# Optimization experiments

Measured on AMD Instinct MI355X. Metric: run time of the kernel, lower is better.

The kernel has to match this reference:

```python
import jax, jax.numpy as jnp
import numpy as np

H = 128      # hidden_size
L = 2        # num_layers
IN0 = 96     # seq_feature_size + context_feature_size
OUT = 1

def _xavier(k, shape):
    fan_out, fan_in = shape
    lim = (6.0 / (fan_in + fan_out)) ** 0.5
    return jax.random.uniform(k, shape, jnp.float32, -lim, lim)

def _orth(k, n):
    q, _ = jnp.linalg.qr(jax.random.normal(k, (n, n)))
    return q.astype(jnp.float32)

def setup_inputs() -> dict:
    key = jax.random.key(0)
    ks = jax.random.split(key, 16)
    B, S, F_seq, F_ctx = 512, 512, 64, 32
    inp = {
        "seq_features": jax.random.normal(ks[0], (B, S, F_seq), jnp.float32),
        "context_features": jax.random.normal(ks[1], (B, F_ctx), jnp.float32),
    }
    for i in range(L):
        in_size = IN0 if i == 0 else H
        inp[f"tau{i}"] = jax.random.normal(ks[2 + 5 * i], (H,), jnp.float32) * 0.1
        inp[f"Win{i}"] = _xavier(ks[3 + 5 * i], (H, in_size))
        inp[f"Wrec{i}"] = _orth(ks[4 + 5 * i], H)
        inp[f"Wg{i}"] = _xavier(ks[5 + 5 * i], (H, in_size + H))
        inp[f"bg{i}"] = jnp.zeros((H,), jnp.float32)
    inp["W1"] = _xavier(ks[12], (H // 2, H))
    inp["b1"] = jnp.zeros((H // 2,), jnp.float32)
    inp["W2"] = _xavier(ks[13], (OUT, H // 2))
    inp["b2"] = jnp.zeros((OUT,), jnp.float32)
    return inp

def _cell_step(x, h, tau_p, Win, Wrec, Wg, bg):
    # LTC cell: RK4 integration of dh/dt = -h/tau + W_in x + gate * W_rec h
    tau = jax.nn.softplus(tau_p) + 1.0
    def rhs(hh):
        gate = jax.nn.sigmoid(jnp.tanh(jnp.concatenate([x, hh], axis=-1) @ Wg.T + bg))
        return -hh / tau + x @ Win.T + gate * (hh @ Wrec.T)
    k1 = rhs(h)
    k2 = rhs(h + 0.5 * k1)
    k3 = rhs(h + 0.5 * k2)
    k4 = rhs(h + k3)
    return jnp.tanh(h + (k1 + 2.0 * k2 + 2.0 * k3 + k4) / 6.0)

def reference(seq_features, context_features, tau0, Win0, Wrec0, Wg0, bg0,
              tau1, Win1, Wrec1, Wg1, bg1, W1, b1, W2, b2):
    B, S, _ = seq_features.shape
    ctx = jnp.broadcast_to(context_features[:, None, :], (B, S, context_features.shape[-1]))
    x = jnp.concatenate([seq_features, ctx], axis=-1)     # [B,S,IN0]
    xs = jnp.swapaxes(x, 0, 1)                            # [S,B,IN0] time-major
    cells = [(tau0, Win0, Wrec0, Wg0, bg0), (tau1, Win1, Wrec1, Wg1, bg1)]
    h_init = tuple(jnp.zeros((B, H), x.dtype) for _ in range(L))

    def step(hs, xt):
        new = []
        inp = xt
        for hi, p in zip(hs, cells):
            hn = _cell_step(inp, hi, *p)
            new.append(hn)
            inp = hn
        return tuple(new), None

    hs, _ = jax.lax.scan(step, h_init, xs)
    h_last = hs[-1]                                       # [B,H]
    # classifier (dropout is identity in eval mode)
    out = jax.nn.sigmoid(jax.nn.relu(h_last @ W1.T + b1) @ W2.T + b2)
    return out.reshape(B, -1)
```

## Files before the change

kernel.cpp:

```cpp
#include <hip/hip_runtime.h>


typedef _Float16 f16;
typedef _Float16 f16x4 __attribute__((ext_vector_type(4)));
typedef _Float16 f16x8 __attribute__((ext_vector_type(8)));
typedef float f32x2 __attribute__((ext_vector_type(2)));
typedef float f32x4 __attribute__((ext_vector_type(4)));

#define NSTEP 512
#define OFF_A0 0
#define OFF_A1 32768
#define OFF_AIO 65536
#define OFF_AX 98304
#define W_TOTAL 122880

#define HQ0 0
#define HQ1 4352
#define L0A 8704
#define L0B 13056
#define L1A 17408
#define L1B 21760
#define L1H 26112
#define XT0 30464
#define XT1 32768
#define SMEM_BYTES 35072

__device__ __forceinline__ float rcp_f(float x) { return __builtin_amdgcn_rcpf(x); }

#define FMA2(A, B, C) __builtin_elementwise_fma((A), (B), (C))
#define B2(X) ((f32x2){(X), (X)})
#define ZERO4 ((f32x4){0.f, 0.f, 0.f, 0.f})
#define ZERO2 ((f32x2){0.f, 0.f})

__device__ __forceinline__ f32x2 tanh2_f(f32x2 z) {
  f32x2 zz = z + z;
  f32x2 e = {__expf(zz[0]), __expf(zz[1])};
  f32x2 d = e + 1.f;
  f32x2 r = {rcp_f(d[0]), rcp_f(d[1])};
  return FMA2(r, B2(-2.f), B2(1.f));
}
__device__ __forceinline__ f32x2 sig2_f(f32x2 t) {
  f32x2 s = t * t;
  f32x2 p = FMA2(s, B2(2.1356861e-5f), B2(-2.1081349e-4f));
  p = FMA2(s, p, B2(2.0833333e-3f));
  p = FMA2(s, p, B2(-2.0833333e-2f));
  p = FMA2(s, p, B2(0.25f));
  return FMA2(t, p, B2(0.5f));
}

#define BAR()                                            \
  do {                                                   \
    asm volatile("s_waitcnt lgkmcnt(0)" ::: "memory");   \
    __builtin_amdgcn_s_barrier();                        \
  } while (0)

__global__ __launch_bounds__(256) void prep_kernel(
    const float* __restrict__ Win0, const float* __restrict__ Wrec0,
    const float* __restrict__ Wg0, const float* __restrict__ Win1,
    const float* __restrict__ Wrec1, const float* __restrict__ Wg1,
    f16* __restrict__ W) {
  int i = blockIdx.x * 256 + threadIdx.x;
  if (i >= W_TOTAL) return;
  if (i < OFF_AX) {
    int sec = i >> 15;
    int r = i & 32767;
    int j = r & 7, lane = (r >> 3) & 63, kc = (r >> 9) & 3, sel = (r >> 11) & 1,
        w = (r >> 12) & 7;
    int row = w * 16 + (lane & 15);
    int k = kc * 32 + ((lane >> 4) << 3) + j;
    float v;
    if (sec == 0)
      v = sel ? Wrec0[row * 128 + k] : Wg0[row * 224 + 96 + k];
    else if (sec == 1)
      v = sel ? Wrec1[row * 128 + k] : Wg1[row * 256 + 128 + k];
    else
      v = sel ? Wg1[row * 256 + k] : Win1[row * 128 + k];
    W[i] = (f16)v;
  } else {
    int r = i - OFF_AX;
    int j = r & 7, lane = (r >> 3) & 63, g = r >> 9;
    int kc = g % 3, sg = g / 3;
    int sel = sg & 1, w = sg >> 1;
    int row = w * 16 + (lane & 15);
    int k = kc * 32 + ((lane >> 4) << 3) + j;
    W[i] = (f16)(sel ? Wg0[row * 224 + k] : Win0[row * 96 + k]);
  }
}

#define MFMA16(A, B, C) __builtin_amdgcn_mfma_f32_16x16x32_f16((A), (B), (C), 0, 0, 0)

#define MM2G(SRC)                                                   \
  {                                                                 \
    ga[0] = gx4[0]; ga[1] = gx4[1];                                 \
    ra[0] = ZERO4; ra[1] = ZERO4;                                   \
    const f16* bp_ = (SRC) + c * 136 + 8 * q;                       \
    _Pragma("unroll") for (int kc_ = 0; kc_ < 4; ++kc_) {           \
      f16x8 bf_ = *(const f16x8*)(bp_ + kc_ * 32);                  \
      ga[0] = MFMA16(awg[0][kc_], bf_, ga[0]);                      \
      ra[0] = MFMA16(awr[0][kc_], bf_, ra[0]);                      \
      ga[1] = MFMA16(awg[1][kc_], bf_, ga[1]);                      \
      ra[1] = MFMA16(awr[1][kc_], bf_, ra[1]);                      \
    }                                                               \
  }

#define MMIO_B(SRC)                                                 \
  {                                                                 \
    ga[0] = ZERO4; ga[1] = ZERO4;                                   \
    ra[0] = bgv4[0]; ra[1] = bgv4[1];                               \
    const f16* bp_ = (SRC) + c * 136 + 8 * q;                       \
    _Pragma("unroll") for (int kc_ = 0; kc_ < 4; ++kc_) {           \
      f16x8 bf_ = *(const f16x8*)(bp_ + kc_ * 32);                  \
      ga[0] = MFMA16(au[0][kc_], bf_, ga[0]);                       \
      ra[0] = MFMA16(ag2[0][kc_], bf_, ra[0]);                      \
      ga[1] = MFMA16(au[1][kc_], bf_, ga[1]);                       \
      ra[1] = MFMA16(ag2[1][kc_], bf_, ra[1]);                      \
    }                                                               \
  }

#define XPROJ(XSRC, UD, GD)                                         \
  {                                                                 \
    f32x4 tg_[2], tr_[2];                                           \
    tg_[0] = ZERO4; tg_[1] = ZERO4;                                 \
    tr_[0] = bgv4[0]; tr_[1] = bgv4[1];                             \
    f16x8 bx0_ = *(const f16x8*)((XSRC) + c * 72 + 8 * q);          \
    f16x8 bx1_ = *(const f16x8*)((XSRC) + c * 72 + 32 + 8 * q);     \
    _Pragma("unroll") for (int i2_ = 0; i2_ < 2; ++i2_) {           \
      tg_[i2_] = MFMA16(au[i2_][0], bx0_, tg_[i2_]);                \
      tr_[i2_] = MFMA16(ag2[i2_][0], bx0_, tr_[i2_]);               \
      tg_[i2_] = MFMA16(au[i2_][1], bx1_, tg_[i2_]);                \
      tr_[i2_] = MFMA16(ag2[i2_][1], bx1_, tr_[i2_]);               \
      tg_[i2_] = MFMA16(au[i2_][2], bctx, tg_[i2_]);                \
      tr_[i2_] = MFMA16(ag2[i2_][2], bctx, tr_[i2_]);               \
      (UD)[i2_] = tg_[i2_];                                         \
      (GD)[i2_] = tr_[i2_];                                         \
    }                                                               \
  }

#define GATEP(WC, HC, DST, FIRST)                                   \
  _Pragma("unroll") for (int i2_ = 0; i2_ < 2; ++i2_) {             \
    f16x4 hv_;                                                      \
    _Pragma("unroll") for (int p_ = 0; p_ < 2; ++p_) {              \
      f32x2 z_ = p_ ? (f32x2){ga[i2_][2], ga[i2_][3]}               \
                    : (f32x2){ga[i2_][0], ga[i2_][1]};              \
      f32x2 rr_ = p_ ? (f32x2){ra[i2_][2], ra[i2_][3]}              \
                     : (f32x2){ra[i2_][0], ra[i2_][1]};             \
      f32x2 th_ = tanh2_f(z_);                                      \
      f32x2 gt_ = sig2_f(th_);                                      \
      f32x2 kk_ = FMA2(gt_, rr_,                                    \
                       FMA2(nitv2[i2_][p_], hhc2[i2_][p_], u2[i2_][p_])); \
      ksum2[i2_][p_] = (FIRST) ? kk_ : FMA2(B2(WC), kk_, ksum2[i2_][p_]); \
      f32x2 hn_ = FMA2(B2(HC), kk_, hst2[i2_][p_]);                 \
      hhc2[i2_][p_] = hn_;                                          \
      hv_[2 * p_] = (f16)hn_[0];                                    \
      hv_[2 * p_ + 1] = (f16)hn_[1];                                \
    }                                                               \
    *(f16x4*)((DST) + c * 136 + jb[i2_]) = hv_;                     \
  }

#define GATEF(DST)                                                  \
  _Pragma("unroll") for (int i2_ = 0; i2_ < 2; ++i2_) {             \
    f16x4 hv_;                                                      \
    _Pragma("unroll") for (int p_ = 0; p_ < 2; ++p_) {              \
      f32x2 z_ = p_ ? (f32x2){ga[i2_][2], ga[i2_][3]}               \
                    : (f32x2){ga[i2_][0], ga[i2_][1]};              \
      f32x2 rr_ = p_ ? (f32x2){ra[i2_][2], ra[i2_][3]}              \
                     : (f32x2){ra[i2_][0], ra[i2_][1]};             \
      f32x2 th_ = tanh2_f(z_);                                      \
      f32x2 gt_ = sig2_f(th_);                                      \
      f32x2 kk_ = FMA2(gt_, rr_,                                    \
                       FMA2(nitv2[i2_][p_], hhc2[i2_][p_], u2[i2_][p_])); \
      f32x2 ks_ = ksum2[i2_][p_] + kk_;                             \
      f32x2 hn_ = tanh2_f(FMA2(B2(0.16666667f), ks_, hst2[i2_][p_])); \
      hst2[i2_][p_] = hn_;                                          \
      hhc2[i2_][p_] = hn_;                                          \
      hv_[2 * p_] = (f16)hn_[0];                                    \
      hv_[2 * p_ + 1] = (f16)hn_[1];                                \
    }                                                               \
    *(f16x4*)((DST) + c * 136 + jb[i2_]) = hv_;                     \
  }

__global__ __launch_bounds__(512, 1) void ltc_kernel(
    const float* __restrict__ seq, const float* __restrict__ ctx,
    const float* __restrict__ tau0p, const float* __restrict__ bg0p,
    const float* __restrict__ tau1p, const float* __restrict__ bg1p,
    const float* __restrict__ W1, const float* __restrict__ b1,
    const float* __restrict__ W2, const float* __restrict__ b2,
    const f16* __restrict__ W, float* __restrict__ out) {
  __shared__ __align__(16) char smem[SMEM_BYTES];
  f16* hq0 = (f16*)(smem + HQ0);
  f16* hq1 = (f16*)(smem + HQ1);
  f16* l0a = (f16*)(smem + L0A);
  f16* l0b = (f16*)(smem + L0B);
  f16* l1a = (f16*)(smem + L1A);
  f16* l1b = (f16*)(smem + L1B);
  f16* l1h = (f16*)(smem + L1H);
  f16* xt0 = (f16*)(smem + XT0);
  f16* xt1 = (f16*)(smem + XT1);

  const int tid = threadIdx.x;
  const int w8 = tid >> 6, lane = tid & 63;
  const int q = lane >> 4, c = lane & 15;
  const int wl = w8 & 3;
  const bool isL0 = (w8 < 4);
  const int bg = blockIdx.x;
  int jb[2];
  jb[0] = 32 * wl + 4 * q;
  jb[1] = jb[0] + 16;

  f16* bufA = isL0 ? l0a : l1a;
  f16* bufB = isL0 ? l0b : l1b;

  f16x8 awg[2][4], awr[2][4], au[2][4], ag2[2][4];
  f16x8 bctx;
  if (isL0) {
#pragma unroll
    for (int i2 = 0; i2 < 2; ++i2) {
      int T = 2 * wl + i2;
#pragma unroll
      for (int kc = 0; kc < 4; ++kc) {
        awg[i2][kc] = *(const f16x8*)(W + OFF_A0 + (((T * 2 + 0) * 4 + kc) * 64 + lane) * 8);
        awr[i2][kc] = *(const f16x8*)(W + OFF_A0 + (((T * 2 + 1) * 4 + kc) * 64 + lane) * 8);
      }
#pragma unroll
      for (int kc = 0; kc < 3; ++kc) {
        au[i2][kc] = *(const f16x8*)(W + OFF_AX + (((T * 2 + 0) * 3 + kc) * 64 + lane) * 8);
        ag2[i2][kc] = *(const f16x8*)(W + OFF_AX + (((T * 2 + 1) * 3 + kc) * 64 + lane) * 8);
      }
      au[i2][3] = (f16x8)(f16)0.f;
      ag2[i2][3] = (f16x8)(f16)0.f;
    }
    const float* cp = ctx + (bg * 16 + c) * 32 + 8 * q;
#pragma unroll
    for (int j = 0; j < 8; ++j) bctx[j] = (f16)cp[j];
  } else {
#pragma unroll
    for (int i2 = 0; i2 < 2; ++i2) {
      int T = 2 * wl + i2;
#pragma unroll
      for (int kc = 0; kc < 4; ++kc) {
        awg[i2][kc] = *(const f16x8*)(W + OFF_A1 + (((T * 2 + 0) * 4 + kc) * 64 + lane) * 8);
        awr[i2][kc] = *(const f16x8*)(W + OFF_A1 + (((T * 2 + 1) * 4 + kc) * 64 + lane) * 8);
        au[i2][kc] = *(const f16x8*)(W + OFF_AIO + (((T * 2 + 0) * 4 + kc) * 64 + lane) * 8);
        ag2[i2][kc] = *(const f16x8*)(W + OFF_AIO + (((T * 2 + 1) * 4 + kc) * 64 + lane) * 8);
      }
    }
  }

  const float* taup = isL0 ? tau0p : tau1p;
  const float* bgp = isL0 ? bg0p : bg1p;
  f32x2 nitv2[2][2];
  f32x4 bgv4[2];
#pragma unroll
  for (int i2 = 0; i2 < 2; ++i2)
#pragma unroll
    for (int r = 0; r < 4; ++r) {
      float t = taup[jb[i2] + r];
      nitv2[i2][r >> 1][r & 1] = -1.f / (logf(1.f + __expf(t)) + 1.f);
      bgv4[i2][r] = bgp[jb[i2] + r];
    }

  f32x2 hst2[2][2], hhc2[2][2], ksum2[2][2], u2[2][2];
  f32x4 ga[2], ra[2], gx4[2], un4[2], gxn4[2];
#pragma unroll
  for (int i2 = 0; i2 < 2; ++i2)
#pragma unroll
    for (int p = 0; p < 2; ++p) {
      hst2[i2][p] = ZERO2;
      hhc2[i2][p] = ZERO2;
      ksum2[i2][p] = ZERO2;
      u2[i2][p] = ZERO2;
    }
  gx4[0] = gx4[1] = ZERO4;
  un4[0] = un4[1] = ZERO4;
  gxn4[0] = gxn4[1] = ZERO4;

  for (int j = tid; j < 2176; j += 512) {
    hq1[j] = (f16)0.f;
    l1h[j] = (f16)0.f;
  }
  const int bs = tid >> 4, fp = tid & 15;
  const size_t seqrow = ((size_t)(bg * 16 + bs)) * NSTEP * 64 + 4 * fp;
  float4 sq_nxt = {0.f, 0.f, 0.f, 0.f};
  float4 sq_ld = sq_nxt;
  if (tid < 256) {
    float4 sv = *(const float4*)(seq + seqrow);
    *(f16x4*)(xt0 + bs * 72 + 4 * fp) =
        (f16x4){(f16)sv.x, (f16)sv.y, (f16)sv.z, (f16)sv.w};
    sq_nxt = *(const float4*)(seq + seqrow + 64);
  }
  __syncthreads();
  if (isL0) {
    XPROJ(xt0, un4, gxn4);
#pragma unroll
    for (int i2 = 0; i2 < 2; ++i2) {
      u2[i2][0] = (f32x2){un4[i2][0], un4[i2][1]};
      u2[i2][1] = (f32x2){un4[i2][2], un4[i2][3]};
      gx4[i2] = gxn4[i2];
    }
  }

#pragma unroll 1
  for (int i = 0; i <= NSTEP; ++i) {
    const f16* hprev = ((i + 1) & 1) ? hq1 : hq0;
    f16* xw = ((i + 1) & 1) ? xt1 : xt0;

    if (isL0) {
      if (i < NSTEP) {
        if (i + 2 < NSTEP)
          sq_ld = *(const float4*)(seq + seqrow + (size_t)(i + 2) * 64);
        MM2G(hprev);
        if (i + 1 < NSTEP)
          *(f16x4*)(xw + bs * 72 + 4 * fp) =
              (f16x4){(f16)sq_nxt.x, (f16)sq_nxt.y, (f16)sq_nxt.z, (f16)sq_nxt.w};
        GATEP(1.0f, 0.5f, bufA, 1);
      }
    } else {
      if (i >= 1) {
        MMIO_B(hprev);
#pragma unroll
        for (int i2 = 0; i2 < 2; ++i2) {
          u2[i2][0] = (f32x2){ga[i2][0], ga[i2][1]};
          u2[i2][1] = (f32x2){ga[i2][2], ga[i2][3]};
          gx4[i2] = ra[i2];
        }
        MM2G(l1h);
        GATEP(1.0f, 0.5f, bufA, 1);
      }
    }
    BAR();

    if (isL0) {
      if (i < NSTEP) {
        MM2G(bufA);
        GATEP(2.0f, 0.5f, bufB, 0);
        if (i + 1 < NSTEP) { XPROJ(xw, un4, gxn4); }
      }
    } else if (i >= 1) {
      MM2G(bufA);
      GATEP(2.0f, 0.5f, bufB, 0);
    }
    BAR();

    if ((isL0 && i < NSTEP) || (!isL0 && i >= 1)) {
      MM2G(bufB);
      GATEP(2.0f, 1.0f, bufA, 0);
    }
    BAR();

    if (isL0) {
      if (i < NSTEP) {
        MM2G(bufA);
        GATEF((i & 1) ? hq1 : hq0);
        if (i + 1 < NSTEP) {
#pragma unroll
          for (int i2 = 0; i2 < 2; ++i2) {
            u2[i2][0] = (f32x2){un4[i2][0], un4[i2][1]};
            u2[i2][1] = (f32x2){un4[i2][2], un4[i2][3]};
            gx4[i2] = gxn4[i2];
          }
          if (i + 2 < NSTEP) sq_nxt = sq_ld;
        }
      }
    } else if (i >= 1) {
      MM2G(bufA);
      GATEF(l1h);
    }
    BAR();
  }

  float* h1f = (float*)smem;
  if (!isL0) {
#pragma unroll
    for (int i2 = 0; i2 < 2; ++i2)
#pragma unroll
      for (int p = 0; p < 2; ++p)
        *(f32x2*)(h1f + c * 132 + jb[i2] + 2 * p) = hst2[i2][p];
  }
  __syncthreads();
  float* z1 = (float*)(smem + 16 * 132 * 4);
  {
    int b = tid >> 5, o = tid & 31;
#pragma unroll
    for (int hlf = 0; hlf < 2; ++hlf) {
      int oo = o + 32 * hlf;
      const float* wr = W1 + oo * 128;
      const float* hr = h1f + b * 132;
      float s = 0.f;
#pragma unroll
      for (int j = 0; j < 128; j += 4) {
        f32x4 wv = *(const f32x4*)(wr + j);
        f32x4 hv = *(const f32x4*)(hr + j);
        s += wv[0] * hv[0] + wv[1] * hv[1] + wv[2] * hv[2] + wv[3] * hv[3];
      }
      s += b1[oo];
      z1[b * 64 + oo] = fmaxf(s, 0.f);
    }
  }
  __syncthreads();
  if (tid < 16) {
    float s = b2[0];
#pragma unroll
    for (int o = 0; o < 64; ++o) s += z1[tid * 64 + o] * W2[o];
    out[bg * 16 + tid] = rcp_f(1.f + __expf(-s));
  }
}

extern "C" void kernel_launch(void* const* d_in, const int* in_sizes, int n_in,
                              void* d_out, int out_size, void* d_ws, size_t ws_size,
                              hipStream_t stream) {
  (void)in_sizes; (void)n_in; (void)out_size; (void)ws_size;
  const float* seq = (const float*)d_in[0];
  const float* ctx = (const float*)d_in[1];
  const float* tau0 = (const float*)d_in[2];
  const float* Win0 = (const float*)d_in[3];
  const float* Wrec0 = (const float*)d_in[4];
  const float* Wg0 = (const float*)d_in[5];
  const float* bg0 = (const float*)d_in[6];
  const float* tau1 = (const float*)d_in[7];
  const float* Win1 = (const float*)d_in[8];
  const float* Wrec1 = (const float*)d_in[9];
  const float* Wg1 = (const float*)d_in[10];
  const float* bg1 = (const float*)d_in[11];
  const float* W1 = (const float*)d_in[12];
  const float* b1 = (const float*)d_in[13];
  const float* W2 = (const float*)d_in[14];
  const float* b2 = (const float*)d_in[15];
  f16* W = (f16*)d_ws;

  prep_kernel<<<480, 256, 0, stream>>>(Win0, Wrec0, Wg0, Win1, Wrec1, Wg1, W);
  ltc_kernel<<<32, 512, 0, stream>>>(seq, ctx, tau0, bg0, tau1, bg1, W1, b1, W2,
                                     b2, W, (float*)d_out);
}
```

Measured before the change: 1.827 ms.

## Double waves per block so each wave owns one 16-row tile

The recurrent kernel goes from 512 to 1024 threads per block, 8 waves per layer instead of 4. Each wave now handles a single 16-row output tile rather than two, which halves the per-wave MFMA chain and register footprint in each RK4 stage. Sequence loads and the classifier are restricted to the original thread subsets. The trade-off is more waves contending at every block barrier and fewer independent MFMA chains per wave to hide latency.

```diff
diff --git a/kernel.cpp b/kernel.cpp
--- a/kernel.cpp
+++ b/kernel.cpp
@@ -91,95 +91,75 @@
 
 #define MM2G(SRC)                                                   \
   {                                                                 \
-    ga[0] = gx4[0]; ga[1] = gx4[1];                                 \
-    ra[0] = ZERO4; ra[1] = ZERO4;                                   \
+    ga = gx4; ra = ZERO4;                                           \
     const f16* bp_ = (SRC) + c * 136 + 8 * q;                       \
     _Pragma("unroll") for (int kc_ = 0; kc_ < 4; ++kc_) {           \
       f16x8 bf_ = *(const f16x8*)(bp_ + kc_ * 32);                  \
-      ga[0] = MFMA16(awg[0][kc_], bf_, ga[0]);                      \
-      ra[0] = MFMA16(awr[0][kc_], bf_, ra[0]);                      \
-      ga[1] = MFMA16(awg[1][kc_], bf_, ga[1]);                      \
-      ra[1] = MFMA16(awr[1][kc_], bf_, ra[1]);                      \
+      ga = MFMA16(awg[kc_], bf_, ga);                               \
+      ra = MFMA16(awr[kc_], bf_, ra);                               \
     }                                                               \
   }
 
 #define MMIO_B(SRC)                                                 \
   {                                                                 \
-    ga[0] = ZERO4; ga[1] = ZERO4;                                   \
-    ra[0] = bgv4[0]; ra[1] = bgv4[1];                               \
+    ga = ZERO4; ra = bgv4;                                          \
     const f16* bp_ = (SRC) + c * 136 + 8 * q;                       \
     _Pragma("unroll") for (int kc_ = 0; kc_ < 4; ++kc_) {           \
       f16x8 bf_ = *(const f16x8*)(bp_ + kc_ * 32);                  \
-      ga[0] = MFMA16(au[0][kc_], bf_, ga[0]);                       \
-      ra[0] = MFMA16(ag2[0][kc_], bf_, ra[0]);                      \
-      ga[1] = MFMA16(au[1][kc_], bf_, ga[1]);                       \
-      ra[1] = MFMA16(ag2[1][kc_], bf_, ra[1]);                      \
+      ga = MFMA16(au[kc_], bf_, ga);                                \
+      ra = MFMA16(ag2[kc_], bf_, ra);                               \
     }                                                               \
   }
 
 #define XPROJ(XSRC, UD, GD)                                         \
   {                                                                 \
-    f32x4 tg_[2], tr_[2];                                           \
-    tg_[0] = ZERO4; tg_[1] = ZERO4;                                 \
-    tr_[0] = bgv4[0]; tr_[1] = bgv4[1];                             \
+    f32x4 tg_ = ZERO4, tr_ = bgv4;                                  \
     f16x8 bx0_ = *(const f16x8*)((XSRC) + c * 72 + 8 * q);          \
     f16x8 bx1_ = *(const f16x8*)((XSRC) + c * 72 + 32 + 8 * q);     \
-    _Pragma("unroll") for (int i2_ = 0; i2_ < 2; ++i2_) {           \
-      tg_[i2_] = MFMA16(au[i2_][0], bx0_, tg_[i2_]);                \
-      tr_[i2_] = MFMA16(ag2[i2_][0], bx0_, tr_[i2_]);               \
-      tg_[i2_] = MFMA16(au[i2_][1], bx1_, tg_[i2_]);                \
-      tr_[i2_] = MFMA16(ag2[i2_][1], bx1_, tr_[i2_]);               \
-      tg_[i2_] = MFMA16(au[i2_][2], bctx, tg_[i2_]);                \
-      tr_[i2_] = MFMA16(ag2[i2_][2], bctx, tr_[i2_]);               \
-      (UD)[i2_] = tg_[i2_];                                         \
-      (GD)[i2_] = tr_[i2_];                                         \
-    }                                                               \
+    tg_ = MFMA16(au[0], bx0_, tg_); tr_ = MFMA16(ag2[0], bx0_, tr_);\
+    tg_ = MFMA16(au[1], bx1_, tg_); tr_ = MFMA16(ag2[1], bx1_, tr_);\
+    tg_ = MFMA16(au[2], bctx, tg_); tr_ = MFMA16(ag2[2], bctx, tr_);\
+    (UD) = tg_; (GD) = tr_;                                         \
   }
 
 #define GATEP(WC, HC, DST, FIRST)                                   \
-  _Pragma("unroll") for (int i2_ = 0; i2_ < 2; ++i2_) {             \
+  {                                                                 \
     f16x4 hv_;                                                      \
     _Pragma("unroll") for (int p_ = 0; p_ < 2; ++p_) {              \
-      f32x2 z_ = p_ ? (f32x2){ga[i2_][2], ga[i2_][3]}               \
-                    : (f32x2){ga[i2_][0], ga[i2_][1]};              \
-      f32x2 rr_ = p_ ? (f32x2){ra[i2_][2], ra[i2_][3]}              \
-                     : (f32x2){ra[i2_][0], ra[i2_][1]};             \
+      f32x2 z_ = {ga[2 * p_], ga[2 * p_ + 1]};                      \
+      f32x2 rr_ = {ra[2 * p_], ra[2 * p_ + 1]};                     \
       f32x2 th_ = tanh2_f(z_);                                      \
       f32x2 gt_ = sig2_f(th_);                                      \
-      f32x2 kk_ = FMA2(gt_, rr_,                                    \
-                       FMA2(nitv2[i2_][p_], hhc2[i2_][p_], u2[i2_][p_])); \
-      ksum2[i2_][p_] = (FIRST) ? kk_ : FMA2(B2(WC), kk_, ksum2[i2_][p_]); \
-      f32x2 hn_ = FMA2(B2(HC), kk_, hst2[i2_][p_]);                 \
-      hhc2[i2_][p_] = hn_;                                          \
+      f32x2 kk_ = FMA2(gt_, rr_, FMA2(nitv2[p_], hhc2[p_], u2[p_])); \
+      ksum2[p_] = (FIRST) ? kk_ : FMA2(B2(WC), kk_, ksum2[p_]);     \
+      f32x2 hn_ = FMA2(B2(HC), kk_, hst2[p_]);                      \
+      hhc2[p_] = hn_;                                               \
       hv_[2 * p_] = (f16)hn_[0];                                    \
       hv_[2 * p_ + 1] = (f16)hn_[1];                                \
     }                                                               \
-    *(f16x4*)((DST) + c * 136 + jb[i2_]) = hv_;                     \
+    *(f16x4*)((DST) + c * 136 + jbase) = hv_;                       \
   }
 
 #define GATEF(DST)                                                  \
-  _Pragma("unroll") for (int i2_ = 0; i2_ < 2; ++i2_) {             \
+  {                                                                 \
     f16x4 hv_;                                                      \
     _Pragma("unroll") for (int p_ = 0; p_ < 2; ++p_) {              \
-      f32x2 z_ = p_ ? (f32x2){ga[i2_][2], ga[i2_][3]}               \
-                    : (f32x2){ga[i2_][0], ga[i2_][1]};              \
-      f32x2 rr_ = p_ ? (f32x2){ra[i2_][2], ra[i2_][3]}              \
-                     : (f32x2){ra[i2_][0], ra[i2_][1]};             \
+      f32x2 z_ = {ga[2 * p_], ga[2 * p_ + 1]};                      \
+      f32x2 rr_ = {ra[2 * p_], ra[2 * p_ + 1]};                     \
       f32x2 th_ = tanh2_f(z_);                                      \
       f32x2 gt_ = sig2_f(th_);                                      \
-      f32x2 kk_ = FMA2(gt_, rr_,                                    \
-                       FMA2(nitv2[i2_][p_], hhc2[i2_][p_], u2[i2_][p_])); \
-      f32x2 ks_ = ksum2[i2_][p_] + kk_;                             \
-      f32x2 hn_ = tanh2_f(FMA2(B2(0.16666667f), ks_, hst2[i2_][p_])); \
-      hst2[i2_][p_] = hn_;                                          \
-      hhc2[i2_][p_] = hn_;                                          \
+      f32x2 kk_ = FMA2(gt_, rr_, FMA2(nitv2[p_], hhc2[p_], u2[p_])); \
+      f32x2 ks_ = ksum2[p_] + kk_;                                  \
+      f32x2 hn_ = tanh2_f(FMA2(B2(0.16666667f), ks_, hst2[p_]));    \
+      hst2[p_] = hn_;                                               \
+      hhc2[p_] = hn_;                                               \
       hv_[2 * p_] = (f16)hn_[0];                                    \
       hv_[2 * p_ + 1] = (f16)hn_[1];                                \
     }                                                               \
-    *(f16x4*)((DST) + c * 136 + jb[i2_]) = hv_;                     \
-  }
-
-__global__ __launch_bounds__(512, 1) void ltc_kernel(
+    *(f16x4*)((DST) + c * 136 + jbase) = hv_;                       \
+  }
+
+__global__ __launch_bounds__(1024, 1) void ltc_kernel(
     const float* __restrict__ seq, const float* __restrict__ ctx,
     const float* __restrict__ tau0p, const float* __restrict__ bg0p,
     const float* __restrict__ tau1p, const float* __restrict__ bg1p,
@@ -198,83 +178,69 @@
   f16* xt1 = (f16*)(smem + XT1);
 
   const int tid = threadIdx.x;
-  const int w8 = tid >> 6, lane = tid & 63;
+  const int w16 = tid >> 6, lane = tid & 63;
   const int q = lane >> 4, c = lane & 15;
-  const int wl = w8 & 3;
-  const bool isL0 = (w8 < 4);
+  const int wl = w16 & 7;
+  const bool isL0 = (w16 < 8);
   const int bg = blockIdx.x;
-  int jb[2];
-  jb[0] = 32 * wl + 4 * q;
-  jb[1] = jb[0] + 16;
+  const int jbase = 16 * wl + 4 * q;
 
   f16* bufA = isL0 ? l0a : l1a;
   f16* bufB = isL0 ? l0b : l1b;
 
-  f16x8 awg[2][4], awr[2][4], au[2][4], ag2[2][4];
-  f16x8 bctx;
+  f16x8 awg[4], awr[4], au[4], ag2[4];
+  f16x8 bctx = (f16x8)(f16)0.f;
   if (isL0) {
 #pragma unroll
-    for (int i2 = 0; i2 < 2; ++i2) {
-      int T = 2 * wl + i2;
-#pragma unroll
-      for (int kc = 0; kc < 4; ++kc) {
-        awg[i2][kc] = *(const f16x8*)(W + OFF_A0 + (((T * 2 + 0) * 4 + kc) * 64 + lane) * 8);
-        awr[i2][kc] = *(const f16x8*)(W + OFF_A0 + (((T * 2 + 1) * 4 + kc) * 64 + lane) * 8);
-      }
-#pragma unroll
-      for (int kc = 0; kc < 3; ++kc) {
-        au[i2][kc] = *(const f16x8*)(W + OFF_AX + (((T * 2 + 0) * 3 + kc) * 64 + lane) * 8);
-        ag2[i2][kc] = *(const f16x8*)(W + OFF_AX + (((T * 2 + 1) * 3 + kc) * 64 + lane) * 8);
-      }
-      au[i2][3] = (f16x8)(f16)0.f;
-      ag2[i2][3] = (f16x8)(f16)0.f;
-    }
+    for (int kc = 0; kc < 4; ++kc) {
+      awg[kc] = *(const f16x8*)(W + OFF_A0 + (((wl * 2 + 0) * 4 + kc) * 64 + lane) * 8);
+      awr[kc] = *(const f16x8*)(W + OFF_A0 + (((wl * 2 + 1) * 4 + kc) * 64 + lane) * 8);
+    }
+#pragma unroll
+    for (int kc = 0; kc < 3; ++kc) {
+      au[kc] = *(const f16x8*)(W + OFF_AX + (((wl * 2 + 0) * 3 + kc) * 64 + lane) * 8);
+      ag2[kc] = *(const f16x8*)(W + OFF_AX + (((wl * 2 + 1) * 3 + kc) * 64 + lane) * 8);
+    }
+    au[3] = (f16x8)(f16)0.f;
+    ag2[3] = (f16x8)(f16)0.f;
     const float* cp = ctx + (bg * 16 + c) * 32 + 8 * q;
 #pragma unroll
     for (int j = 0; j < 8; ++j) bctx[j] = (f16)cp[j];
   } else {
 #pragma unroll
-    for (int i2 = 0; i2 < 2; ++i2) {
-      int T = 2 * wl + i2;
-#pragma unroll
-      for (int kc = 0; kc < 4; ++kc) {
-        awg[i2][kc] = *(const f16x8*)(W + OFF_A1 + (((T * 2 + 0) * 4 + kc) * 64 + lane) * 8);
-        awr[i2][kc] = *(const f16x8*)(W + OFF_A1 + (((T * 2 + 1) * 4 + kc) * 64 + lane) * 8);
-        au[i2][kc] = *(const f16x8*)(W + OFF_AIO + (((T * 2 + 0) * 4 + kc) * 64 + lane) * 8);
-        ag2[i2][kc] = *(const f16x8*)(W + OFF_AIO + (((T * 2 + 1) * 4 + kc) * 64 + lane) * 8);
-      }
+    for (int kc = 0; kc < 4; ++kc) {
+      awg[kc] = *(const f16x8*)(W + OFF_A1 + (((wl * 2 + 0) * 4 + kc) * 64 + lane) * 8);
+      awr[kc] = *(const f16x8*)(W + OFF_A1 + (((wl * 2 + 1) * 4 + kc) * 64 + lane) * 8);
+      au[kc] = *(const f16x8*)(W + OFF_AIO + (((wl * 2 + 0) * 4 + kc) * 64 + lane) * 8);
+      ag2[kc] = *(const f16x8*)(W + OFF_AIO + (((wl * 2 + 1) * 4 + kc) * 64 + lane) * 8);
     }
   }
 
   const float* taup = isL0 ? tau0p : tau1p;
   const float* bgp = isL0 ? bg0p : bg1p;
-  f32x2 nitv2[2][2];
-  f32x4 bgv4[2];
-#pragma unroll
-  for (int i2 = 0; i2 < 2; ++i2)
-#pragma unroll
-    for (int r = 0; r < 4; ++r) {
-      float t = taup[jb[i2] + r];
-      nitv2[i2][r >> 1][r & 1] = -1.f / (logf(1.f + __expf(t)) + 1.f);
-      bgv4[i2][r] = bgp[jb[i2] + r];
-    }
-
-  f32x2 hst2[2][2], hhc2[2][2], ksum2[2][2], u2[2][2];
-  f32x4 ga[2], ra[2], gx4[2], un4[2], gxn4[2];
-#pragma unroll
-  for (int i2 = 0; i2 < 2; ++i2)
-#pragma unroll
-    for (int p = 0; p < 2; ++p) {
-      hst2[i2][p] = ZERO2;
-      hhc2[i2][p] = ZERO2;
-      ksum2[i2][p] = ZERO2;
-      u2[i2][p] = ZERO2;
-    }
-  gx4[0] = gx4[1] = ZERO4;
-  un4[0] = un4[1] = ZERO4;
-  gxn4[0] = gxn4[1] = ZERO4;
-
-  for (int j = tid; j < 2176; j += 512) {
+  f32x2 nitv2[2];
+  f32x4 bgv4;
+#pragma unroll
+  for (int r = 0; r < 4; ++r) {
+    float t = taup[jbase + r];
+    nitv2[r >> 1][r & 1] = -1.f / (logf(1.f + __expf(t)) + 1.f);
+    bgv4[r] = bgp[jbase + r];
+  }
+
+  f32x2 hst2[2], hhc2[2], ksum2[2], u2[2];
+  f32x4 ga, ra, gx4, un4, gxn4;
+#pragma unroll
+  for (int p = 0; p < 2; ++p) {
+    hst2[p] = ZERO2;
+    hhc2[p] = ZERO2;
+    ksum2[p] = ZERO2;
+    u2[p] = ZERO2;
+  }
+  gx4 = ZERO4;
+  un4 = ZERO4;
+  gxn4 = ZERO4;
+
+  for (int j = tid; j < 2176; j += 1024) {
     hq1[j] = (f16)0.f;
     l1h[j] = (f16)0.f;
   }
@@ -291,12 +257,9 @@
   __syncthreads();
   if (isL0) {
     XPROJ(xt0, un4, gxn4);
-#pragma unroll
-    for (int i2 = 0; i2 < 2; ++i2) {
-      u2[i2][0] = (f32x2){un4[i2][0], un4[i2][1]};
-      u2[i2][1] = (f32x2){un4[i2][2], un4[i2][3]};
-      gx4[i2] = gxn4[i2];
-    }
+    u2[0] = (f32x2){un4[0], un4[1]};
+    u2[1] = (f32x2){un4[2], un4[3]};
+    gx4 = gxn4;
   }
 
 #pragma unroll 1
@@ -306,10 +269,10 @@
 
     if (isL0) {
       if (i < NSTEP) {
-        if (i + 2 < NSTEP)
+        if (tid < 256 && i + 2 < NSTEP)
           sq_ld = *(const float4*)(seq + seqrow + (size_t)(i + 2) * 64);
         MM2G(hprev);
-        if (i + 1 < NSTEP)
+        if (tid < 256 && i + 1 < NSTEP)
           *(f16x4*)(xw + bs * 72 + 4 * fp) =
               (f16x4){(f16)sq_nxt.x, (f16)sq_nxt.y, (f16)sq_nxt.z, (f16)sq_nxt.w};
         GATEP(1.0f, 0.5f, bufA, 1);
@@ -317,12 +280,9 @@
     } else {
       if (i >= 1) {
         MMIO_B(hprev);
-#pragma unroll
-        for (int i2 = 0; i2 < 2; ++i2) {
-          u2[i2][0] = (f32x2){ga[i2][0], ga[i2][1]};
-          u2[i2][1] = (f32x2){ga[i2][2], ga[i2][3]};
-          gx4[i2] = ra[i2];
-        }
+        u2[0] = (f32x2){ga[0], ga[1]};
+        u2[1] = (f32x2){ga[2], ga[3]};
+        gx4 = ra;
         MM2G(l1h);
         GATEP(1.0f, 0.5f, bufA, 1);
       }
@@ -352,12 +312,9 @@
         MM2G(bufA);
         GATEF((i & 1) ? hq1 : hq0);
         if (i + 1 < NSTEP) {
-#pragma unroll
-          for (int i2 = 0; i2 < 2; ++i2) {
-            u2[i2][0] = (f32x2){un4[i2][0], un4[i2][1]};
-            u2[i2][1] = (f32x2){un4[i2][2], un4[i2][3]};
-            gx4[i2] = gxn4[i2];
-          }
+          u2[0] = (f32x2){un4[0], un4[1]};
+          u2[1] = (f32x2){un4[2], un4[3]};
+          gx4 = gxn4;
           if (i + 2 < NSTEP) sq_nxt = sq_ld;
         }
       }
@@ -371,29 +328,29 @@
   float* h1f = (float*)smem;
   if (!isL0) {
 #pragma unroll
-    for (int i2 = 0; i2 < 2; ++i2)
-#pragma unroll
-      for (int p = 0; p < 2; ++p)
-        *(f32x2*)(h1f + c * 132 + jb[i2] + 2 * p) = hst2[i2][p];
+    for (int p = 0; p < 2; ++p)
+      *(f32x2*)(h1f + c * 132 + jbase + 2 * p) = hst2[p];
   }
   __syncthreads();
   float* z1 = (float*)(smem + 16 * 132 * 4);
   {
     int b = tid >> 5, o = tid & 31;
-#pragma unroll
-    for (int hlf = 0; hlf < 2; ++hlf) {
-      int oo = o + 32 * hlf;
-      const float* wr = W1 + oo * 128;
-      const float* hr = h1f + b * 132;
-      float s = 0.f;
-#pragma unroll
-      for (int j = 0; j < 128; j += 4) {
-        f32x4 wv = *(const f32x4*)(wr + j);
-        f32x4 hv = *(const f32x4*)(hr + j);
-        s += wv[0] * hv[0] + wv[1] * hv[1] + wv[2] * hv[2] + wv[3] * hv[3];
-      }
-      s += b1[oo];
-      z1[b * 64 + oo] = fmaxf(s, 0.f);
+    if (b < 16) {
+#pragma unroll
+      for (int hlf = 0; hlf < 2; ++hlf) {
+        int oo = o + 32 * hlf;
+        const float* wr = W1 + oo * 128;
+        const float* hr = h1f + b * 132;
+        float s = 0.f;
+#pragma unroll
+        for (int j = 0; j < 128; j += 4) {
+          f32x4 wv = *(const f32x4*)(wr + j);
+          f32x4 hv = *(const f32x4*)(hr + j);
+          s += wv[0] * hv[0] + wv[1] * hv[1] + wv[2] * hv[2] + wv[3] * hv[3];
+        }
+        s += b1[oo];
+        z1[b * 64 + oo] = fmaxf(s, 0.f);
+      }
     }
   }
   __syncthreads();
@@ -428,6 +385,6 @@
   f16* W = (f16*)d_ws;
 
   prep_kernel<<<480, 256, 0, stream>>>(Win0, Wrec0, Wg0, Win1, Wrec1, Wg1, W);
-  ltc_kernel<<<32, 512, 0, stream>>>(seq, ctx, tau0, bg0, tau1, bg1, W1, b1, W2,
-                                     b2, W, (float*)d_out);
-}
+  ltc_kernel<<<32, 1024, 0, stream>>>(seq, ctx, tau0, bg0, tau1, bg1, W1, b1,
+                                      W2, b2, W, (float*)d_out);
+}
```

New measurement: 2.761 ms. 1.51x slower.
